# Optimization experiments

Hardware: AMD Instinct MI355X
Metric: run time of the kernel (lower is better)

Reference implementation:

```python
import jax, jax.numpy as jnp
import numpy as np
import math

B, S, H, OUT = 8, 2048, 512, 512
NQ, NL = 8, 3            # num_qubits, num_layers
NP = NQ // 2             # entangled pairs = 4
PS = H // NP             # pair size = 128
NS = NQ                  # superposition states = 8

_H2 = jnp.array([[1.0, 1.0], [1.0, -1.0]], jnp.float32) / math.sqrt(2.0)
_PX = jnp.array([[0.0, 1.0], [1.0, 0.0]], jnp.float32)
_PZ = jnp.array([[1.0, 0.0], [0.0, -1.0]], jnp.float32)
_CNOT = jnp.array([[1, 0, 0, 0], [0, 1, 0, 0], [0, 0, 0, 1], [0, 0, 1, 0]], jnp.float32)


def _gate2(x, m):
    # apply a 2x2 gate to consecutive pairs along the last dim
    shp = x.shape
    return (x.reshape(shp[:-1] + (shp[-1] // 2, 2)) @ m).reshape(shp)


def _cnot(x):
    # apply 4x4 CNOT to consecutive quadruples along the last dim
    shp = x.shape
    return (x.reshape(shp[:-1] + (shp[-1] // 4, 4)) @ _CNOT).reshape(shp)


def setup_inputs() -> dict:
    key = jax.random.key(0)
    ks = jax.random.split(key, 8)
    x = jax.random.normal(ks[0], (B, S, H), jnp.float32)
    in_W = jax.random.normal(ks[1], (H, H), jnp.float32) / math.sqrt(H)
    in_b = jnp.zeros((H,), jnp.float32)
    ent_W = jax.random.normal(ks[2], (NP, PS, PS), jnp.float32) * 0.1
    ent_strength = jnp.ones((NP,), jnp.float32)
    sup_W = jax.random.normal(ks[3], (NS, H), jnp.float32) * 0.1
    sup_coeffs = jnp.ones((NS,), jnp.float32) / math.sqrt(NS)
    circuit_params = jax.random.normal(ks[4], (NL, NQ, 3), jnp.float32) * 0.1
    meas_ops = jnp.eye(H, dtype=jnp.float32)  # 'computational' basis
    out_W = jax.random.normal(ks[5], (H, OUT), jnp.float32) / math.sqrt(H)
    out_b = jnp.zeros((OUT,), jnp.float32)
    return dict(x=x, in_W=in_W, in_b=in_b, ent_W=ent_W, ent_strength=ent_strength,
                sup_W=sup_W, sup_coeffs=sup_coeffs, circuit_params=circuit_params,
                meas_ops=meas_ops, out_W=out_W, out_b=out_b)


def reference(x, in_W, in_b, ent_W, ent_strength, sup_W, sup_coeffs,
              circuit_params, meas_ops, out_W, out_b):
    # input projection
    x = x @ in_W + in_b

    # quantum entanglement: per-pair linear map + CNOT + strength scale
    xp = x.reshape(B, S, NP, PS)
    xp = jnp.einsum('bspi,pij->bspj', xp, ent_W)
    xp = _cnot(xp) * ent_strength[None, None, :, None]
    x = xp.reshape(B, S, H)

    # quantum superposition: the Hadamard gate is identical across states,
    # so sum_i coeff_i * w_i * Had(x) = Had(x) * sum_i coeff_i * w_i
    x = _gate2(x, _H2) * jnp.einsum('s,sh->h', sup_coeffs, sup_W)

    # variational circuit layers
    rep = H // NQ  # tile per-qubit params across hidden
    for layer in range(NL):
        x = _gate2(x, _H2)
        px = jnp.repeat(circuit_params[layer, :, 0], rep)
        x = x + px * _gate2(x, _PX)
        # Pauli-Y branch: (x + 0j) @ [[0,-i],[i,0]] is purely imaginary ->
        # its real part is exactly zero; faithful no-op (zero grads too)
        pz = jnp.repeat(circuit_params[layer, :, 2], rep)
        x = x + pz * _gate2(x, _PZ)
        x = _cnot(x)

    # measurement (computational basis) + output projection
    x = x @ meas_ops
    return x @ out_W + out_b


if __name__ == '__main__':
    out = reference(**setup_inputs())
    print(out.shape, out.dtype)
```

## Files before the change

kernel.cpp:

```cpp
#include <hip/hip_runtime.h>
#include <hip/hip_bf16.h>


typedef float  fvec4 __attribute__((ext_vector_type(4)));
typedef float  f32x4 __attribute__((ext_vector_type(4)));
typedef short  short8 __attribute__((ext_vector_type(8)));
typedef unsigned short us8 __attribute__((ext_vector_type(8)));
typedef unsigned short us4 __attribute__((ext_vector_type(4)));

#define H 512
#define NL 3

__device__ __forceinline__ unsigned short f2bf(float f) {
    return __bfloat16_as_ushort(__float2bfloat16(f));
}
__device__ __forceinline__ void gll16(const void* g, void* l) {
    __builtin_amdgcn_global_load_lds((const __attribute__((address_space(1))) void*)g,
                                     (__attribute__((address_space(3))) void*)l, 16, 0, 0);
}

__global__ __launch_bounds__(512) void k_prep(const float* __restrict__ in_W,
                                              const float* __restrict__ in_b,
                                              const float* __restrict__ entW,
                                              const float* __restrict__ strength,
                                              const float* __restrict__ supW,
                                              const float* __restrict__ coeffs,
                                              const float* __restrict__ cp,
                                              float* __restrict__ W1f,
                                              float* __restrict__ bmid) {
    __shared__ float sseg[H];
    __shared__ float sval[H];
    __shared__ float sw[H];
    const int r = blockIdx.x;
    const int tid = threadIdx.x;
    const float* src = (r < H) ? (in_W + (size_t)r * H) : in_b;
    float* dst = (r < H) ? (W1f + (size_t)r * H) : bmid;

    sseg[tid] = src[tid];
    float wacc = 0.f;
#pragma unroll
    for (int s = 0; s < 8; ++s) wacc += coeffs[s] * supW[s * H + tid];
    sw[tid] = wacc;
    __syncthreads();

    const int p = tid >> 7, j = tid & 127;
    const int jsrc = (j & 2) ? (j ^ 1) : j;
    const float* wcol = entW + p * (128 * 128) + jsrc;
    const float* seg = sseg + p * 128;
    float acc = 0.f;
#pragma unroll 8
    for (int i = 0; i < 128; ++i) acc += seg[i] * wcol[i * 128];
    acc *= strength[p];
    __syncthreads();
    sval[tid] = acc;
    __syncthreads();

    const int q4 = tid & ~3;
    float v0 = sval[q4], v1 = sval[q4 + 1], v2 = sval[q4 + 2], v3 = sval[q4 + 3];
    const float is2 = 0.70710678118654752440f;
    float t0, t1, t2, t3;
    t0 = (v0 + v1) * is2; t1 = (v0 - v1) * is2;
    t2 = (v2 + v3) * is2; t3 = (v2 - v3) * is2;
    v0 = t0 * sw[q4]; v1 = t1 * sw[q4 + 1]; v2 = t2 * sw[q4 + 2]; v3 = t3 * sw[q4 + 3];
    const int qb = tid >> 6;
#pragma unroll
    for (int l = 0; l < NL; ++l) {
        float px = cp[l * 24 + qb * 3 + 0];
        float pz = cp[l * 24 + qb * 3 + 2];
        t0 = (v0 + v1) * is2; t1 = (v0 - v1) * is2;
        t2 = (v2 + v3) * is2; t3 = (v2 - v3) * is2;
        v0 = t0; v1 = t1; v2 = t2; v3 = t3;
        t0 = v0 + px * v1; t1 = v1 + px * v0;
        t2 = v2 + px * v3; t3 = v3 + px * v2;
        v0 = t0; v1 = t1; v2 = t2; v3 = t3;
        v0 *= (1.f + pz); v1 *= (1.f - pz);
        v2 *= (1.f + pz); v3 *= (1.f - pz);
        t0 = v2; v2 = v3; v3 = t0;
    }
    const int pos = tid & 3;
    dst[tid] = (pos == 0) ? v0 : (pos == 1) ? v1 : (pos == 2) ? v2 : v3;
}

__global__ __launch_bounds__(512) void k_mid(const float* __restrict__ W1f,
                                             const float* __restrict__ outW,
                                             const float* __restrict__ bmid,
                                             const float* __restrict__ outb,
                                             unsigned short* __restrict__ MtotT,
                                             float* __restrict__ btot) {
    __shared__ __align__(16) char smem[131072];
    const int bx = blockIdx.x;
    const int tid = threadIdx.x;

    if (bx < 64) {
        char* As = smem;
        char* Bs = smem + 65536;
        const int bm = (bx >> 3) * 64, bn = (bx & 7) * 64;

#pragma unroll
        for (int i = 0; i < 8; ++i) {
            int c = i * 512 + tid;
            int rr = c >> 6, kc = (c & 63) * 8;
            const float* s = W1f + (size_t)(bm + rr) * H + kc;
            fvec4 a0 = *(const fvec4*)s, a1 = *(const fvec4*)(s + 4);
            us8 hv;
            hv[0] = f2bf(a0.x); hv[1] = f2bf(a0.y); hv[2] = f2bf(a0.z); hv[3] = f2bf(a0.w);
            hv[4] = f2bf(a1.x); hv[5] = f2bf(a1.y); hv[6] = f2bf(a1.z); hv[7] = f2bf(a1.w);
            *(us8*)(As + ((rr * 1024 + kc * 2) ^ ((rr & 7) << 4))) = hv;
        }
#pragma unroll
        for (int i = 0; i < 16; ++i) {
            int c = i * 512 + tid;
            int k = c >> 4, n4 = (c & 15) * 4;
            fvec4 v = *(const fvec4*)(outW + (size_t)k * H + bn + n4);
#pragma unroll
            for (int jj = 0; jj < 4; ++jj) {
                int n = n4 + jj;
                *(unsigned short*)(Bs + ((n * 1024 + k * 2) ^ ((n & 7) << 4))) =
                    f2bf(jj == 0 ? v.x : jj == 1 ? v.y : jj == 2 ? v.z : v.w);
            }
        }
        __syncthreads();

        const int lane = tid & 63, wid = tid >> 6;
        const int wm = wid >> 2, wn = wid & 3;
        const int ro = lane & 15, ko8 = (lane >> 4) * 8;
        f32x4 acc0 = (f32x4)0.f, acc1 = (f32x4)0.f;
#pragma unroll
        for (int kk = 0; kk < 16; ++kk) {
            const int kb = (kk * 32 + ko8) * 2;
            int r0 = wm * 32 + ro, r1 = r0 + 16, rn = wn * 16 + ro;
            short8 af0 = *(const short8*)(As + ((r0 * 1024 + kb) ^ ((r0 & 7) << 4)));
            short8 af1 = *(const short8*)(As + ((r1 * 1024 + kb) ^ ((r1 & 7) << 4)));
            short8 bfr = *(const short8*)(Bs + ((rn * 1024 + kb) ^ ((rn & 7) << 4)));
            acc0 = __builtin_amdgcn_mfma_f32_16x16x32_bf16(af0, bfr, acc0, 0, 0, 0);
            acc1 = __builtin_amdgcn_mfma_f32_16x16x32_bf16(af1, bfr, acc1, 0, 0, 0);
        }
        const int crow = (lane >> 4) * 4, ccol = lane & 15;
        const int gcol = bn + wn * 16 + ccol;
        {
            us4 hv;
            hv[0] = f2bf(acc0[0]); hv[1] = f2bf(acc0[1]);
            hv[2] = f2bf(acc0[2]); hv[3] = f2bf(acc0[3]);
            *(us4*)(MtotT + (size_t)gcol * H + bm + wm * 32 + crow) = hv;
            hv[0] = f2bf(acc1[0]); hv[1] = f2bf(acc1[1]);
            hv[2] = f2bf(acc1[2]); hv[3] = f2bf(acc1[3]);
            *(us4*)(MtotT + (size_t)gcol * H + bm + wm * 32 + 16 + crow) = hv;
        }
    } else {
        float a0 = 0.f, a1 = 0.f, a2 = 0.f, a3 = 0.f;
#pragma unroll 4
        for (int h = 0; h < H; h += 4) {
            a0 += bmid[h + 0] * outW[(size_t)(h + 0) * H + tid];
            a1 += bmid[h + 1] * outW[(size_t)(h + 1) * H + tid];
            a2 += bmid[h + 2] * outW[(size_t)(h + 2) * H + tid];
            a3 += bmid[h + 3] * outW[(size_t)(h + 3) * H + tid];
        }
        btot[tid] = outb[tid] + ((a0 + a1) + (a2 + a3));
    }
}

__global__ __launch_bounds__(512) void k_main(const float* __restrict__ A,
                                              const unsigned short* __restrict__ Bt,
                                              float* __restrict__ C,
                                              const float* __restrict__ bias) {
    __shared__ __align__(16) unsigned short As[2][64 * 64];
    __shared__ __align__(16) unsigned short Bs[2][512 * 64];
    const int tid = threadIdx.x;
    const int bm = blockIdx.x * 64;
    const int lane = tid & 63, wid = tid >> 6;
    const int ro = lane & 15, ko8 = (lane >> 4) * 8;

    const int arr = tid >> 3, akc = (tid & 7) * 8;
    const float* aptr = A + (size_t)(bm + arr) * H + akc;
    const int awoff = ((arr * 128 + akc * 2) ^ ((arr & 7) << 4));

    const int brow = tid >> 3;
    const char* bbase = (const char*)Bt + (size_t)brow * 1024 +
                        (((tid & 7) * 16) ^ ((brow & 7) << 4));
    const int bdst = wid * 1024;

    f32x4 acc[4][4];
#pragma unroll
    for (int i = 0; i < 4; ++i)
#pragma unroll
        for (int j = 0; j < 4; ++j) acc[i][j] = (f32x4)0.f;

    {
        fvec4 a0 = *(const fvec4*)aptr, a1 = *(const fvec4*)(aptr + 4);
#pragma unroll
        for (int i = 0; i < 8; ++i)
            gll16(bbase + (size_t)i * 65536, (char*)&Bs[0][0] + i * 8192 + bdst);
        us8 hv;
        hv[0] = f2bf(a0.x); hv[1] = f2bf(a0.y); hv[2] = f2bf(a0.z); hv[3] = f2bf(a0.w);
        hv[4] = f2bf(a1.x); hv[5] = f2bf(a1.y); hv[6] = f2bf(a1.z); hv[7] = f2bf(a1.w);
        *(us8*)((char*)&As[0][0] + awoff) = hv;
    }
    __syncthreads();

    for (int t = 0; t < 8; ++t) {
        const int buf = t & 1;
        fvec4 pa0, pa1;
        if (t < 7) {
            pa0 = *(const fvec4*)(aptr + (t + 1) * 64);
            pa1 = *(const fvec4*)(aptr + (t + 1) * 64 + 4);
#pragma unroll
            for (int i = 0; i < 8; ++i)
                gll16(bbase + (size_t)i * 65536 + (t + 1) * 128,
                      (char*)&Bs[buf ^ 1][0] + i * 8192 + bdst);
        }
#pragma unroll
        for (int kk = 0; kk < 2; ++kk) {
            short8 af[4], bfr[4];
#pragma unroll
            for (int am = 0; am < 4; ++am) {
                int row = am * 16 + ro;
                af[am] = *(const short8*)((const char*)&As[buf][0] +
                         ((row * 128 + (kk * 32 + ko8) * 2) ^ ((row & 7) << 4)));
            }
#pragma unroll
            for (int bj = 0; bj < 4; ++bj) {
                int row = wid * 64 + bj * 16 + ro;
                bfr[bj] = *(const short8*)((const char*)&Bs[buf][0] +
                          ((row * 128 + (kk * 32 + ko8) * 2) ^ ((row & 7) << 4)));
            }
#pragma unroll
            for (int am = 0; am < 4; ++am)
#pragma unroll
                for (int bj = 0; bj < 4; ++bj)
                    acc[am][bj] = __builtin_amdgcn_mfma_f32_16x16x32_bf16(af[am], bfr[bj], acc[am][bj], 0, 0, 0);
        }
        if (t < 7) {
            us8 hv;
            hv[0] = f2bf(pa0.x); hv[1] = f2bf(pa0.y); hv[2] = f2bf(pa0.z); hv[3] = f2bf(pa0.w);
            hv[4] = f2bf(pa1.x); hv[5] = f2bf(pa1.y); hv[6] = f2bf(pa1.z); hv[7] = f2bf(pa1.w);
            *(us8*)((char*)&As[buf ^ 1][0] + awoff) = hv;
        }
        __syncthreads();
    }

    const int crow = (lane >> 4) * 4, ccol = lane & 15;
#pragma unroll
    for (int am = 0; am < 4; ++am)
#pragma unroll
        for (int bj = 0; bj < 4; ++bj) {
            const int gcol = wid * 64 + bj * 16 + ccol;
            const float bv = bias[gcol];
            const int grow = bm + am * 16 + crow;
#pragma unroll
            for (int j = 0; j < 4; ++j)
                C[(size_t)(grow + j) * H + gcol] = acc[am][bj][j] + bv;
        }
}

extern "C" void kernel_launch(void* const* d_in, const int* in_sizes, int n_in,
                              void* d_out, int out_size, void* d_ws, size_t ws_size,
                              hipStream_t stream) {
    const float* x      = (const float*)d_in[0];
    const float* in_W   = (const float*)d_in[1];
    const float* in_b   = (const float*)d_in[2];
    const float* ent_W  = (const float*)d_in[3];
    const float* ent_s  = (const float*)d_in[4];
    const float* sup_W  = (const float*)d_in[5];
    const float* sup_c  = (const float*)d_in[6];
    const float* cp     = (const float*)d_in[7];
    const float* out_W  = (const float*)d_in[9];
    const float* out_b  = (const float*)d_in[10];
    float* out = (float*)d_out;

    char* ws = (char*)d_ws;
    const size_t MB = 1u << 20;
    if (ws_size < 16384 + MB + MB) return;

    float* bmid = (float*)(ws);
    float* btot = (float*)(ws + 4096);
    float* W1f  = (float*)(ws + 16384);
    unsigned short* MtotT = (unsigned short*)(ws + 16384 + MB);

    k_prep<<<dim3(513), dim3(512), 0, stream>>>(in_W, in_b, ent_W, ent_s,
                                                sup_W, sup_c, cp, W1f, bmid);
    k_mid<<<dim3(65), dim3(512), 0, stream>>>(W1f, out_W, bmid, out_b, MtotT, btot);
    k_main<<<dim3(256), dim3(512), 0, stream>>>(x, MtotT, out, btot);
}
```

Before: 46.97 us.

## Fuse weight-prep kernels into one MFMA build kernel and prefetch x into cache

Merges the per-row prep kernel and the mid GEMM kernel into one launch, k_build. Each of its 64 tile blocks computes its slice of the entanglement matmul with bf16 MFMA, then applies the Hadamard and circuit transforms in LDS before the out_W product. This removes the fp32 W1f round trip through global memory and one kernel launch. A single block computes the folded bias. The remaining 191 blocks stream x so it is already cached when k_main runs. The costs are redundant entanglement work across the 8 column blocks of each row band, and bf16 rounding of the entanglement matmul inputs, which was fp32 before.

Result: slower. 70.95 us (+51.1%).

```diff
diff --git a/kernel.cpp b/kernel.cpp
--- a/kernel.cpp
+++ b/kernel.cpp
@@ -19,94 +19,120 @@
                                      (__attribute__((address_space(3))) void*)l, 16, 0, 0);
 }
 
-__global__ __launch_bounds__(512) void k_prep(const float* __restrict__ in_W,
-                                              const float* __restrict__ in_b,
-                                              const float* __restrict__ entW,
-                                              const float* __restrict__ strength,
-                                              const float* __restrict__ supW,
-                                              const float* __restrict__ coeffs,
-                                              const float* __restrict__ cp,
-                                              float* __restrict__ W1f,
-                                              float* __restrict__ bmid) {
-    __shared__ float sseg[H];
-    __shared__ float sval[H];
-    __shared__ float sw[H];
-    const int r = blockIdx.x;
-    const int tid = threadIdx.x;
-    const float* src = (r < H) ? (in_W + (size_t)r * H) : in_b;
-    float* dst = (r < H) ? (W1f + (size_t)r * H) : bmid;
-
-    sseg[tid] = src[tid];
-    float wacc = 0.f;
-#pragma unroll
-    for (int s = 0; s < 8; ++s) wacc += coeffs[s] * supW[s * H + tid];
-    sw[tid] = wacc;
-    __syncthreads();
-
-    const int p = tid >> 7, j = tid & 127;
-    const int jsrc = (j & 2) ? (j ^ 1) : j;
-    const float* wcol = entW + p * (128 * 128) + jsrc;
-    const float* seg = sseg + p * 128;
-    float acc = 0.f;
-#pragma unroll 8
-    for (int i = 0; i < 128; ++i) acc += seg[i] * wcol[i * 128];
-    acc *= strength[p];
-    __syncthreads();
-    sval[tid] = acc;
-    __syncthreads();
-
-    const int q4 = tid & ~3;
-    float v0 = sval[q4], v1 = sval[q4 + 1], v2 = sval[q4 + 2], v3 = sval[q4 + 3];
-    const float is2 = 0.70710678118654752440f;
-    float t0, t1, t2, t3;
-    t0 = (v0 + v1) * is2; t1 = (v0 - v1) * is2;
-    t2 = (v2 + v3) * is2; t3 = (v2 - v3) * is2;
-    v0 = t0 * sw[q4]; v1 = t1 * sw[q4 + 1]; v2 = t2 * sw[q4 + 2]; v3 = t3 * sw[q4 + 3];
-    const int qb = tid >> 6;
-#pragma unroll
-    for (int l = 0; l < NL; ++l) {
-        float px = cp[l * 24 + qb * 3 + 0];
-        float pz = cp[l * 24 + qb * 3 + 2];
-        t0 = (v0 + v1) * is2; t1 = (v0 - v1) * is2;
-        t2 = (v2 + v3) * is2; t3 = (v2 - v3) * is2;
-        v0 = t0; v1 = t1; v2 = t2; v3 = t3;
-        t0 = v0 + px * v1; t1 = v1 + px * v0;
-        t2 = v2 + px * v3; t3 = v3 + px * v2;
-        v0 = t0; v1 = t1; v2 = t2; v3 = t3;
-        v0 *= (1.f + pz); v1 *= (1.f - pz);
-        v2 *= (1.f + pz); v3 *= (1.f - pz);
-        t0 = v2; v2 = v3; v3 = t0;
-    }
-    const int pos = tid & 3;
-    dst[tid] = (pos == 0) ? v0 : (pos == 1) ? v1 : (pos == 2) ? v2 : v3;
-}
-
-__global__ __launch_bounds__(512) void k_mid(const float* __restrict__ W1f,
-                                             const float* __restrict__ outW,
-                                             const float* __restrict__ bmid,
-                                             const float* __restrict__ outb,
-                                             unsigned short* __restrict__ MtotT,
-                                             float* __restrict__ btot) {
+__global__ __launch_bounds__(512) void k_build(
+        const float* __restrict__ x, const float* __restrict__ in_W,
+        const float* __restrict__ in_b, const float* __restrict__ entW,
+        const float* __restrict__ strength, const float* __restrict__ supW,
+        const float* __restrict__ coeffs, const float* __restrict__ cp,
+        const float* __restrict__ outW, const float* __restrict__ outb,
+        unsigned short* __restrict__ MtotT, float* __restrict__ btot) {
     __shared__ __align__(16) char smem[131072];
     const int bx = blockIdx.x;
     const int tid = threadIdx.x;
+    const float is2 = 0.70710678118654752440f;
 
     if (bx < 64) {
-        char* As = smem;
-        char* Bs = smem + 65536;
+        char*  As = smem;
+        float* A1 = (float*)(smem + 65536);
+        float* sw = (float*)(smem + 65536 + 33792);
+        char*  Bs = smem + 65536;
+
         const int bm = (bx >> 3) * 64, bn = (bx & 7) * 64;
-
-#pragma unroll
-        for (int i = 0; i < 8; ++i) {
-            int c = i * 512 + tid;
-            int rr = c >> 6, kc = (c & 63) * 8;
-            const float* s = W1f + (size_t)(bm + rr) * H + kc;
-            fvec4 a0 = *(const fvec4*)s, a1 = *(const fvec4*)(s + 4);
-            us8 hv;
-            hv[0] = f2bf(a0.x); hv[1] = f2bf(a0.y); hv[2] = f2bf(a0.z); hv[3] = f2bf(a0.w);
-            hv[4] = f2bf(a1.x); hv[5] = f2bf(a1.y); hv[6] = f2bf(a1.z); hv[7] = f2bf(a1.w);
-            *(us8*)(As + ((rr * 1024 + kc * 2) ^ ((rr & 7) << 4))) = hv;
-        }
+        const int lane = tid & 63, wid = tid >> 6;
+        const int wm = wid >> 2, wn = wid & 3;
+        const int ro = lane & 15, ko8 = (lane >> 4) * 8;
+        const int crow = (lane >> 4) * 4, ccol = lane & 15;
+
+        {
+            float wacc = 0.f;
+#pragma unroll
+            for (int s = 0; s < 8; ++s) wacc += coeffs[s] * supW[s * H + tid];
+            sw[tid] = wacc;
+        }
+
+        for (int p = 0; p < 4; ++p) {
+            short8 paf[2][4], pbf[2][4];
+#pragma unroll
+            for (int am = 0; am < 2; ++am)
+#pragma unroll
+                for (int ks = 0; ks < 4; ++ks) {
+                    const int row = bm + wm * 32 + am * 16 + ro;
+                    const float* ap = in_W + (size_t)row * H + p * 128 + ks * 32 + ko8;
+                    fvec4 a0 = *(const fvec4*)ap, a1 = *(const fvec4*)(ap + 4);
+                    short8 h;
+                    h[0] = (short)f2bf(a0.x); h[1] = (short)f2bf(a0.y);
+                    h[2] = (short)f2bf(a0.z); h[3] = (short)f2bf(a0.w);
+                    h[4] = (short)f2bf(a1.x); h[5] = (short)f2bf(a1.y);
+                    h[6] = (short)f2bf(a1.z); h[7] = (short)f2bf(a1.w);
+                    paf[am][ks] = h;
+                }
+#pragma unroll
+            for (int nt = 0; nt < 2; ++nt)
+#pragma unroll
+                for (int ks = 0; ks < 4; ++ks) {
+                    const int colp = wn * 32 + nt * 16 + ro;
+                    const int jsrc = (colp & 2) ? (colp ^ 1) : colp;
+                    const float* bp = entW + p * 16384 + (ks * 32 + ko8) * 128 + jsrc;
+                    short8 h;
+#pragma unroll
+                    for (int e = 0; e < 8; ++e) h[e] = (short)f2bf(bp[e * 128]);
+                    pbf[nt][ks] = h;
+                }
+            f32x4 pacc[2][2];
+            pacc[0][0] = (f32x4)0.f; pacc[0][1] = (f32x4)0.f;
+            pacc[1][0] = (f32x4)0.f; pacc[1][1] = (f32x4)0.f;
+#pragma unroll
+            for (int ks = 0; ks < 4; ++ks)
+#pragma unroll
+                for (int am = 0; am < 2; ++am)
+#pragma unroll
+                    for (int nt = 0; nt < 2; ++nt)
+                        pacc[am][nt] = __builtin_amdgcn_mfma_f32_16x16x32_bf16(
+                            paf[am][ks], pbf[nt][ks], pacc[am][nt], 0, 0, 0);
+            const float st = strength[p];
+#pragma unroll
+            for (int am = 0; am < 2; ++am)
+#pragma unroll
+                for (int nt = 0; nt < 2; ++nt)
+#pragma unroll
+                    for (int j = 0; j < 4; ++j)
+                        A1[(wm * 32 + am * 16 + crow + j) * 132 +
+                           (wn * 32 + nt * 16 + ccol)] = pacc[am][nt][j] * st;
+            __syncthreads();
+#pragma unroll
+            for (int it = 0; it < 4; ++it) {
+                const int qi = it * 512 + tid;
+                const int r = qi >> 5, qc = (qi & 31) * 4;
+                const int gc = p * 128 + qc;
+                float v0 = A1[r * 132 + qc + 0], v1 = A1[r * 132 + qc + 1];
+                float v2 = A1[r * 132 + qc + 2], v3 = A1[r * 132 + qc + 3];
+                float t0, t1, t2, t3;
+                t0 = (v0 + v1) * is2; t1 = (v0 - v1) * is2;
+                t2 = (v2 + v3) * is2; t3 = (v2 - v3) * is2;
+                v0 = t0 * sw[gc]; v1 = t1 * sw[gc + 1];
+                v2 = t2 * sw[gc + 2]; v3 = t3 * sw[gc + 3];
+                const int qb = gc >> 6;
+#pragma unroll
+                for (int l = 0; l < NL; ++l) {
+                    float px = cp[l * 24 + qb * 3 + 0];
+                    float pz = cp[l * 24 + qb * 3 + 2];
+                    t0 = (v0 + v1) * is2; t1 = (v0 - v1) * is2;
+                    t2 = (v2 + v3) * is2; t3 = (v2 - v3) * is2;
+                    v0 = t0; v1 = t1; v2 = t2; v3 = t3;
+                    t0 = v0 + px * v1; t1 = v1 + px * v0;
+                    t2 = v2 + px * v3; t3 = v3 + px * v2;
+                    v0 = t0; v1 = t1; v2 = t2; v3 = t3;
+                    v0 *= (1.f + pz); v1 *= (1.f - pz);
+                    v2 *= (1.f + pz); v3 *= (1.f - pz);
+                    t0 = v2; v2 = v3; v3 = t0;
+                }
+                us4 hv;
+                hv[0] = f2bf(v0); hv[1] = f2bf(v1); hv[2] = f2bf(v2); hv[3] = f2bf(v3);
+                *(us4*)(As + ((r * 1024 + gc * 2) ^ ((r & 7) << 4))) = hv;
+            }
+            __syncthreads();
+        }
+
 #pragma unroll
         for (int i = 0; i < 16; ++i) {
             int c = i * 512 + tid;
@@ -121,9 +147,6 @@
         }
         __syncthreads();
 
-        const int lane = tid & 63, wid = tid >> 6;
-        const int wm = wid >> 2, wn = wid & 3;
-        const int ro = lane & 15, ko8 = (lane >> 4) * 8;
         f32x4 acc0 = (f32x4)0.f, acc1 = (f32x4)0.f;
 #pragma unroll
         for (int kk = 0; kk < 16; ++kk) {
@@ -135,27 +158,73 @@
             acc0 = __builtin_amdgcn_mfma_f32_16x16x32_bf16(af0, bfr, acc0, 0, 0, 0);
             acc1 = __builtin_amdgcn_mfma_f32_16x16x32_bf16(af1, bfr, acc1, 0, 0, 0);
         }
-        const int crow = (lane >> 4) * 4, ccol = lane & 15;
         const int gcol = bn + wn * 16 + ccol;
-        {
-            us4 hv;
-            hv[0] = f2bf(acc0[0]); hv[1] = f2bf(acc0[1]);
-            hv[2] = f2bf(acc0[2]); hv[3] = f2bf(acc0[3]);
-            *(us4*)(MtotT + (size_t)gcol * H + bm + wm * 32 + crow) = hv;
-            hv[0] = f2bf(acc1[0]); hv[1] = f2bf(acc1[1]);
-            hv[2] = f2bf(acc1[2]); hv[3] = f2bf(acc1[3]);
-            *(us4*)(MtotT + (size_t)gcol * H + bm + wm * 32 + 16 + crow) = hv;
-        }
+        us4 hv;
+        hv[0] = f2bf(acc0[0]); hv[1] = f2bf(acc0[1]);
+        hv[2] = f2bf(acc0[2]); hv[3] = f2bf(acc0[3]);
+        *(us4*)(MtotT + (size_t)gcol * H + bm + wm * 32 + crow) = hv;
+        hv[0] = f2bf(acc1[0]); hv[1] = f2bf(acc1[1]);
+        hv[2] = f2bf(acc1[2]); hv[3] = f2bf(acc1[3]);
+        *(us4*)(MtotT + (size_t)gcol * H + bm + wm * 32 + 16 + crow) = hv;
+
+    } else if (bx == 64) {
+        float* sseg = (float*)smem;
+        float* sval = sseg + 512;
+        float* swb  = sval + 512;
+        sseg[tid] = in_b[tid];
+        float wacc = 0.f;
+#pragma unroll
+        for (int s = 0; s < 8; ++s) wacc += coeffs[s] * supW[s * H + tid];
+        swb[tid] = wacc;
+        __syncthreads();
+        const int p = tid >> 7, j = tid & 127;
+        const int jsrc = (j & 2) ? (j ^ 1) : j;
+        const float* wcol = entW + p * 16384 + jsrc;
+        float acc = 0.f;
+#pragma unroll 8
+        for (int i = 0; i < 128; ++i) acc += sseg[p * 128 + i] * wcol[i * 128];
+        acc *= strength[p];
+        __syncthreads();
+        sval[tid] = acc;
+        __syncthreads();
+        const int q4 = tid & ~3;
+        float v0 = sval[q4], v1 = sval[q4 + 1], v2 = sval[q4 + 2], v3 = sval[q4 + 3];
+        float t0, t1, t2, t3;
+        t0 = (v0 + v1) * is2; t1 = (v0 - v1) * is2;
+        t2 = (v2 + v3) * is2; t3 = (v2 - v3) * is2;
+        v0 = t0 * swb[q4]; v1 = t1 * swb[q4 + 1];
+        v2 = t2 * swb[q4 + 2]; v3 = t3 * swb[q4 + 3];
+        const int qb = tid >> 6;
+#pragma unroll
+        for (int l = 0; l < NL; ++l) {
+            float px = cp[l * 24 + qb * 3 + 0];
+            float pz = cp[l * 24 + qb * 3 + 2];
+            t0 = (v0 + v1) * is2; t1 = (v0 - v1) * is2;
+            t2 = (v2 + v3) * is2; t3 = (v2 - v3) * is2;
+            v0 = t0; v1 = t1; v2 = t2; v3 = t3;
+            t0 = v0 + px * v1; t1 = v1 + px * v0;
+            t2 = v2 + px * v3; t3 = v3 + px * v2;
+            v0 = t0; v1 = t1; v2 = t2; v3 = t3;
+            v0 *= (1.f + pz); v1 *= (1.f - pz);
+            v2 *= (1.f + pz); v3 *= (1.f - pz);
+            t0 = v2; v2 = v3; v3 = t0;
+        }
+        const int pos = tid & 3;
+        __syncthreads();
+        sseg[tid] = (pos == 0) ? v0 : (pos == 1) ? v1 : (pos == 2) ? v2 : v3;
+        __syncthreads();
+        float a0 = outb[tid];
+#pragma unroll 4
+        for (int h = 0; h < H; ++h) a0 += sseg[h] * outW[(size_t)h * H + tid];
+        btot[tid] = a0;
+
     } else {
-        float a0 = 0.f, a1 = 0.f, a2 = 0.f, a3 = 0.f;
-#pragma unroll 4
-        for (int h = 0; h < H; h += 4) {
-            a0 += bmid[h + 0] * outW[(size_t)(h + 0) * H + tid];
-            a1 += bmid[h + 1] * outW[(size_t)(h + 1) * H + tid];
-            a2 += bmid[h + 2] * outW[(size_t)(h + 2) * H + tid];
-            a3 += bmid[h + 3] * outW[(size_t)(h + 3) * H + tid];
-        }
-        btot[tid] = outb[tid] + ((a0 + a1) + (a2 + a3));
+        const int pb = bx - 65;
+        const fvec4* xv = (const fvec4*)x;
+        for (size_t i = (size_t)pb * 512 + tid; i < 2097152u; i += 191u * 512u) {
+            fvec4 v = xv[i];
+            asm volatile("" :: "v"(v.x), "v"(v.y), "v"(v.z), "v"(v.w));
+        }
     }
 }
 
@@ -268,16 +337,13 @@
     float* out = (float*)d_out;
 
     char* ws = (char*)d_ws;
-    const size_t MB = 1u << 20;
-    if (ws_size < 16384 + MB + MB) return;
-
-    float* bmid = (float*)(ws);
-    float* btot = (float*)(ws + 4096);
-    float* W1f  = (float*)(ws + 16384);
-    unsigned short* MtotT = (unsigned short*)(ws + 16384 + MB);
-
-    k_prep<<<dim3(513), dim3(512), 0, stream>>>(in_W, in_b, ent_W, ent_s,
-                                                sup_W, sup_c, cp, W1f, bmid);
-    k_mid<<<dim3(65), dim3(512), 0, stream>>>(W1f, out_W, bmid, out_b, MtotT, btot);
+    if (ws_size < 4096 + H * H * sizeof(unsigned short)) return;
+
+    float* btot = (float*)(ws);
+    unsigned short* MtotT = (unsigned short*)(ws + 4096);
+
+    k_build<<<dim3(256), dim3(512), 0, stream>>>(x, in_W, in_b, ent_W, ent_s,
+                                                 sup_W, sup_c, cp, out_W, out_b,
+                                                 MtotT, btot);
     k_main<<<dim3(256), dim3(512), 0, stream>>>(x, MtotT, out, btot);
 }
```
